# Kernel tuning notes

Hardware: AMD Instinct MI355X
Metric: run time of the kernel (lower is better)

Reference implementation:

```python
import jax, jax.numpy as jnp
import numpy as np

N_NODES = 100000
N_EDGES = 1600000
IN_FEATS, HID_FEATS, OUT_FEATS = 64, 64, 32


def setup_inputs() -> dict:
    key = jax.random.key(0)
    ks = jax.random.split(key, 8)
    x = jax.random.normal(ks[0], (N_NODES, IN_FEATS), dtype=jnp.float32)
    edge_index = jax.random.randint(ks[1], (2, N_EDGES), 0, N_NODES, dtype=jnp.int64)
    s1 = 1.0 / np.sqrt(IN_FEATS)
    s2 = 1.0 / np.sqrt(HID_FEATS)
    return {
        "x": x,
        "edge_index": edge_index,
        "W1l": jax.random.uniform(ks[2], (IN_FEATS, HID_FEATS), jnp.float32, -s1, s1),
        "W1r": jax.random.uniform(ks[3], (IN_FEATS, HID_FEATS), jnp.float32, -s1, s1),
        "b1": jnp.zeros((HID_FEATS,), jnp.float32),
        "W2l": jax.random.uniform(ks[4], (HID_FEATS, OUT_FEATS), jnp.float32, -s2, s2),
        "W2r": jax.random.uniform(ks[5], (HID_FEATS, OUT_FEATS), jnp.float32, -s2, s2),
        "b2": jnp.zeros((OUT_FEATS,), jnp.float32),
    }


def _mean_aggregate(h, src, dst, n_nodes):
    # gather source features, scatter-mean into destination nodes
    msg_sum = jax.ops.segment_sum(h[src], dst, num_segments=n_nodes)  # [N, D]
    cnt = jax.ops.segment_sum(jnp.ones(src.shape, h.dtype), dst, num_segments=n_nodes)
    return msg_sum / jnp.maximum(cnt, 1.0)[:, None]  # zero in-degree -> 0


def _sage_conv(h, src, dst, Wl, Wr, b):
    # PyG SAGEConv: lin_l(mean_j x_j) + lin_r(x_i); bias lives in lin_l
    agg = _mean_aggregate(h, src, dst, h.shape[0])
    return agg @ Wl + h @ Wr + b


def reference(x, edge_index, W1l, W1r, b1, W2l, W2r, b2):
    src, dst = edge_index[0], edge_index[1]
    h = jax.nn.relu(_sage_conv(x, src, dst, W1l, W1r, b1))
    out = _sage_conv(h, src, dst, W2l, W2r, b2)
    return out
```

## Files before the change

### kernel.cpp

```cpp
#include <hip/hip_runtime.h>

#define NN 100000
#define NE 1600000
#define NBK 392
#define CAPB 6144
#define CVTB 6250

typedef __attribute__((ext_vector_type(8))) short bf16x8;
typedef __attribute__((ext_vector_type(4))) float f32x4;

__device__ __forceinline__ unsigned short f2b(float f) {
  unsigned b = __float_as_uint(f);
  unsigned r = b + 0x7FFF + ((b >> 16) & 1);
  return (unsigned short)(r >> 16);
}

__global__ void k_zero(int* __restrict__ g) {
  if (threadIdx.x < NBK) g[threadIdx.x] = 0;
}

__global__ void k_pre(const float* __restrict__ x, unsigned short* __restrict__ xb,
                      const float* __restrict__ W1l, const float* __restrict__ W1r,
                      unsigned short* __restrict__ WT1,
                      const float* __restrict__ W2l, const float* __restrict__ W2r,
                      unsigned short* __restrict__ WT2,
                      const int* __restrict__ src, const int* __restrict__ dst,
                      int* __restrict__ gcur, unsigned* __restrict__ pairbuf) {
  __shared__ int hist[NBK];
  __shared__ int sc[512];
  __shared__ int base[NBK], lofs[NBK];
  __shared__ unsigned epk[4096];
  __shared__ unsigned short ebk[4096];
  int t = threadIdx.x;
  int b = blockIdx.x;
  if (b < CVTB) {
    int i = (b * 256 + t) * 4;
    float4 v = *(const float4*)(x + i);
    ushort4 o;
    o.x = f2b(v.x); o.y = f2b(v.y); o.z = f2b(v.z); o.w = f2b(v.w);
    *(ushort4*)(xb + i) = o;
    return;
  }
  if (b == CVTB) {
    for (int i = t; i < 64 * 128; i += 256) {
      int f = i >> 7, k = i & 127;
      WT1[i] = f2b((k < 64) ? W1l[k * 64 + f] : W1r[(k - 64) * 64 + f]);
    }
    return;
  }
  if (b == CVTB + 1) {
    for (int i = t; i < 32 * 128; i += 256) {
      int f = i >> 7, k = i & 127;
      WT2[i] = f2b((k < 64) ? W2l[k * 32 + f] : W2r[(k - 64) * 32 + f]);
    }
    return;
  }
  int pb = b - (CVTB + 2);
  for (int i = t; i < NBK; i += 256) { hist[i] = 0; lofs[i] = 0; }
  __syncthreads();
  unsigned pk[16]; int bk[16];
  int e0 = pb * 4096 + t;
#pragma unroll
  for (int j = 0; j < 16; ++j) {
    int e = e0 + j * 256;
    if (e < NE) {
      int d = dst[e], s = src[e];
      bk[j] = d >> 8;
      pk[j] = ((unsigned)s << 8) | (unsigned)(d & 255);
      atomicAdd(&hist[bk[j]], 1);
    } else bk[j] = -1;
  }
  __syncthreads();
  sc[t] = (t < NBK) ? hist[t] : 0;
  sc[t + 256] = (t + 256 < NBK) ? hist[t + 256] : 0;
  __syncthreads();
  for (int off = 1; off < 512; off <<= 1) {
    int v0 = (t >= off) ? sc[t - off] : 0;
    int v1 = sc[t + 256 - off];
    __syncthreads();
    sc[t] += v0;
    sc[t + 256] += v1;
    __syncthreads();
  }
  for (int i = t; i < NBK; i += 256) {
    int h = hist[i];
    base[i] = atomicAdd(&gcur[i], h);
    hist[i] = sc[i] - h;
  }
  __syncthreads();
#pragma unroll
  for (int j = 0; j < 16; ++j) {
    if (bk[j] >= 0) {
      int pos = hist[bk[j]] + atomicAdd(&lofs[bk[j]], 1);
      epk[pos] = pk[j];
      ebk[pos] = (unsigned short)bk[j];
    }
  }
  __syncthreads();
  int cb = sc[511];
  for (int i = t; i < cb; i += 256) {
    unsigned p = epk[i];
    int bb = ebk[i];
    int slot = base[bb] + (i - hist[bb]);
    if (slot < CAPB) pairbuf[(size_t)bb * CAPB + slot] = p;
  }
}

__global__ void k_partB(const unsigned* __restrict__ pairbuf, const int* __restrict__ gcur,
                        int* __restrict__ esrc, uint2* __restrict__ rowp2) {
  __shared__ int cnt[256], cur[256], ssum[256];
  __shared__ int ebuf[CAPB];
  int b = blockIdx.x, t = threadIdx.x;
  int cb = gcur[b]; if (cb > CAPB) cb = CAPB;
  if (t < 256) cnt[t] = 0;
  __syncthreads();
  const unsigned* pb = pairbuf + (size_t)b * CAPB;
  for (int i = t; i < cb; i += 512) atomicAdd(&cnt[pb[i] & 255], 1);
  __syncthreads();
  int a0 = (t < 256) ? cnt[t] : 0;
  if (t < 256) ssum[t] = a0;
  __syncthreads();
  for (int off = 1; off < 256; off <<= 1) {
    int tmp = (t < 256 && t >= off) ? ssum[t - off] : 0;
    __syncthreads();
    if (t < 256) ssum[t] += tmp;
    __syncthreads();
  }
  if (t < 256) {
    int ex = ssum[t] - a0;
    cur[t] = ex;
    int n = b * 256 + t;
    if (n < NN) rowp2[n] = make_uint2((unsigned)(b * CAPB + ex),
                                      (unsigned)(b * CAPB + ex + a0));
  }
  __syncthreads();
  for (int i = t; i < cb; i += 512) {
    unsigned p = pb[i];
    int pos = atomicAdd(&cur[p & 255], 1);
    ebuf[pos] = (int)(p >> 8);
  }
  __syncthreads();
  for (int i = t; i < cb; i += 512) esrc[(size_t)b * CAPB + i] = ebuf[i];
}

__global__ __launch_bounds__(256, 4) void k_agg(
    const uint2* __restrict__ fb64, const uint2* __restrict__ rowp2,
    const int* __restrict__ esrc, uint2* __restrict__ aggb64) {
  int tid = blockIdx.x * 256 + threadIdx.x;
  int node = tid >> 4;
  int c16 = tid & 15;
  int qbase = threadIdx.x & 48;
  unsigned long long rp =
      __builtin_nontemporal_load((const unsigned long long*)&rowp2[node]);
  int beg = (int)(unsigned)rp;
  int deg = (int)(unsigned)(rp >> 32) - beg;
  float a0 = 0.f, a1 = 0.f, a2 = 0.f, a3 = 0.f;

  int nfull = deg & ~15;
  for (int r0 = 0; r0 < nfull; r0 += 16) {
    int idxv = __builtin_nontemporal_load(&esrc[beg + r0 + c16]);
    int sv[16];
#pragma unroll
    for (int j = 0; j < 16; ++j) sv[j] = __shfl(idxv, qbase + j);
    uint2 v[16];
#pragma unroll
    for (int j = 0; j < 16; ++j) v[j] = fb64[(size_t)sv[j] * 16 + c16];
    __builtin_amdgcn_sched_barrier(0);
#pragma unroll
    for (int j = 0; j < 16; ++j) {
      a0 += __uint_as_float(v[j].x << 16);
      a1 += __uint_as_float(v[j].x & 0xFFFF0000u);
      a2 += __uint_as_float(v[j].y << 16);
      a3 += __uint_as_float(v[j].y & 0xFFFF0000u);
    }
  }
  int rem = deg - nfull;
  if (rem) {
    int idxv = __builtin_nontemporal_load(&esrc[beg + nfull + (c16 < rem ? c16 : 0)]);
    int sv[16];
#pragma unroll
    for (int j = 0; j < 16; ++j) sv[j] = __shfl(idxv, qbase + j);
    uint2 v[16];
#pragma unroll
    for (int j = 0; j < 16; ++j)
      if (j < rem) v[j] = fb64[(size_t)sv[j] * 16 + c16];
    __builtin_amdgcn_sched_barrier(0);
#pragma unroll
    for (int j = 0; j < 16; ++j)
      if (j < rem) {
        a0 += __uint_as_float(v[j].x << 16);
        a1 += __uint_as_float(v[j].x & 0xFFFF0000u);
        a2 += __uint_as_float(v[j].y << 16);
        a3 += __uint_as_float(v[j].y & 0xFFFF0000u);
      }
  }
  float inv = (deg > 0) ? (1.0f / (float)deg) : 0.f;
  uint2 o;
  o.x = (unsigned)f2b(a0 * inv) | ((unsigned)f2b(a1 * inv) << 16);
  o.y = (unsigned)f2b(a2 * inv) | ((unsigned)f2b(a3 * inv) << 16);
  aggb64[(size_t)node * 16 + c16] = o;
}

template <int NF>
__global__ __launch_bounds__(256) void k_gemm(
    const unsigned short* __restrict__ aggb, const unsigned short* __restrict__ featb,
    const unsigned short* __restrict__ WT, const float* __restrict__ bias,
    float* __restrict__ out, unsigned short* __restrict__ ob, int relu) {
  __shared__ unsigned short As[64 * 128];
  __shared__ unsigned short Ws[NF * 128];
  int tid = threadIdx.x;
  int n0 = blockIdx.x * 64;
  int lane = tid & 63, wr = tid >> 6;

  for (int cch = tid; cch < 64 * 16; cch += 256) {
    int r = cch >> 4, s = cch & 15;
    int n = n0 + r;
    bf16x8 v = {0, 0, 0, 0, 0, 0, 0, 0};
    if (n < NN) {
      const unsigned short* p = (s < 8) ? (aggb + (size_t)n * 64 + s * 8)
                                        : (featb + (size_t)n * 64 + (s - 8) * 8);
      v = *(const bf16x8*)p;
    }
    *(bf16x8*)(&As[r * 128 + ((s ^ (r & 15)) << 3)]) = v;
  }
  for (int cch = tid; cch < NF * 16; cch += 256) {
    int f = cch >> 4, s = cch & 15;
    bf16x8 v = *(const bf16x8*)(WT + f * 128 + s * 8);
    *(bf16x8*)(&Ws[f * 128 + ((s ^ (f & 15)) << 3)]) = v;
  }
  __syncthreads();

  int l15 = lane & 15, lg = lane >> 4;
  int arow = wr * 16 + l15;
  f32x4 acc[NF / 16];
#pragma unroll
  for (int ct = 0; ct < NF / 16; ++ct) acc[ct] = (f32x4){0.f, 0.f, 0.f, 0.f};

#pragma unroll
  for (int k0 = 0; k0 < 4; ++k0) {
    int sa = k0 * 4 + lg;
    bf16x8 a = *(const bf16x8*)(&As[arow * 128 + ((sa ^ (arow & 15)) << 3)]);
#pragma unroll
    for (int ct = 0; ct < NF / 16; ++ct) {
      int bcol = ct * 16 + l15;
      bf16x8 b = *(const bf16x8*)(&Ws[bcol * 128 + ((sa ^ (bcol & 15)) << 3)]);
      acc[ct] = __builtin_amdgcn_mfma_f32_16x16x32_bf16(a, b, acc[ct], 0, 0, 0);
    }
  }

#pragma unroll
  for (int ct = 0; ct < NF / 16; ++ct) {
    int f = ct * 16 + l15;
    float bv = bias[f];
#pragma unroll
    for (int r = 0; r < 4; ++r) {
      int n = n0 + wr * 16 + lg * 4 + r;
      if (n >= NN) continue;
      float v = acc[ct][r] + bv;
      if (relu) v = fmaxf(v, 0.f);
      if (out) out[(size_t)n * NF + f] = v;
      if (ob) ob[(size_t)n * NF + f] = f2b(v);
    }
  }
}

extern "C" void kernel_launch(void* const* d_in, const int* in_sizes, int n_in,
                              void* d_out, int out_size, void* d_ws, size_t ws_size,
                              hipStream_t stream) {
  const float* x   = (const float*)d_in[0];
  const int*   ei  = (const int*)d_in[1];
  const float* W1l = (const float*)d_in[2];
  const float* W1r = (const float*)d_in[3];
  const float* b1  = (const float*)d_in[4];
  const float* W2l = (const float*)d_in[5];
  const float* W2r = (const float*)d_in[6];
  const float* b2  = (const float*)d_in[7];
  const int* src = ei;
  const int* dst = ei + NE;
  float* out = (float*)d_out;

  char* ws = (char*)d_ws;
  size_t off = 0;
  auto take = [&](size_t bytes) -> char* {
    char* p = ws + off;
    off = (off + bytes + 255) & ~(size_t)255;
    return p;
  };
  int*      gcur    = (int*)take((size_t)NBK * 4);
  unsigned* pairbuf = (unsigned*)take((size_t)NBK * CAPB * 4);
  int*      esrc    = (int*)take((size_t)NBK * CAPB * 4);
  uint2*    rowp2   = (uint2*)take((size_t)NN * 8);
  unsigned short* aggb = (unsigned short*)take((size_t)NN * 64 * 2);
  unsigned short* xb   = (unsigned short*)take((size_t)NN * 64 * 2);
  unsigned short* hb   = (unsigned short*)take((size_t)NN * 64 * 2);
  unsigned short* WT1  = (unsigned short*)take((size_t)64 * 128 * 2);
  unsigned short* WT2  = (unsigned short*)take((size_t)32 * 128 * 2);

  int nbA = (NE + 4095) / 4096;
  k_zero<<<1, 512, 0, stream>>>(gcur);
  k_pre<<<CVTB + 2 + nbA, 256, 0, stream>>>(x, xb, W1l, W1r, WT1, W2l, W2r, WT2,
                                            src, dst, gcur, pairbuf);
  k_partB<<<NBK, 512, 0, stream>>>(pairbuf, gcur, esrc, rowp2);

  int nbG = (NN + 63) / 64;
  k_agg<<<NN / 16, 256, 0, stream>>>((const uint2*)xb, rowp2, esrc, (uint2*)aggb);
  k_gemm<64><<<nbG, 256, 0, stream>>>(aggb, xb, WT1, b1, nullptr, hb, 1);
  k_agg<<<NN / 16, 256, 0, stream>>>((const uint2*)hb, rowp2, esrc, (uint2*)aggb);
  k_gemm<32><<<nbG, 256, 0, stream>>>(aggb, hb, WT2, b2, out, nullptr, 0);
}
```

Measured before the change: 131.0 us.

## Split bf16 feature tables into two 32-column slabs for cache-friendly gathers

Measured after the change: 159.0 us. 21.4% more time.

```diff
diff --git a/kernel.cpp b/kernel.cpp
--- a/kernel.cpp
+++ b/kernel.cpp
@@ -5,6 +5,7 @@
 #define NBK 392
 #define CAPB 6144
 #define CVTB 6250
+#define SLABU (NN * 32)
 
 typedef __attribute__((ext_vector_type(8))) short bf16x8;
 typedef __attribute__((ext_vector_type(4))) float f32x4;
@@ -35,10 +36,11 @@
   int b = blockIdx.x;
   if (b < CVTB) {
     int i = (b * 256 + t) * 4;
+    int n = i >> 6, f = i & 63;
     float4 v = *(const float4*)(x + i);
     ushort4 o;
     o.x = f2b(v.x); o.y = f2b(v.y); o.z = f2b(v.z); o.w = f2b(v.w);
-    *(ushort4*)(xb + i) = o;
+    *(ushort4*)(xb + (size_t)(f >> 5) * SLABU + (size_t)n * 32 + (f & 31)) = o;
     return;
   }
   if (b == CVTB) {
@@ -144,30 +146,30 @@
 }
 
 __global__ __launch_bounds__(256, 4) void k_agg(
-    const uint2* __restrict__ fb64, const uint2* __restrict__ rowp2,
-    const int* __restrict__ esrc, uint2* __restrict__ aggb64) {
+    const uint2* __restrict__ slab_fb, const uint2* __restrict__ rowp2,
+    const int* __restrict__ esrc, uint2* __restrict__ slab_out) {
   int tid = blockIdx.x * 256 + threadIdx.x;
-  int node = tid >> 4;
-  int c16 = tid & 15;
-  int qbase = threadIdx.x & 48;
+  int node = tid >> 3;
+  int c8 = tid & 7;
+  int gbase = threadIdx.x & 56;
   unsigned long long rp =
       __builtin_nontemporal_load((const unsigned long long*)&rowp2[node]);
   int beg = (int)(unsigned)rp;
   int deg = (int)(unsigned)(rp >> 32) - beg;
   float a0 = 0.f, a1 = 0.f, a2 = 0.f, a3 = 0.f;
 
-  int nfull = deg & ~15;
-  for (int r0 = 0; r0 < nfull; r0 += 16) {
-    int idxv = __builtin_nontemporal_load(&esrc[beg + r0 + c16]);
-    int sv[16];
-#pragma unroll
-    for (int j = 0; j < 16; ++j) sv[j] = __shfl(idxv, qbase + j);
-    uint2 v[16];
-#pragma unroll
-    for (int j = 0; j < 16; ++j) v[j] = fb64[(size_t)sv[j] * 16 + c16];
+  int nfull = deg & ~7;
+  for (int r0 = 0; r0 < nfull; r0 += 8) {
+    int idxv = __builtin_nontemporal_load(&esrc[beg + r0 + c8]);
+    int sv[8];
+#pragma unroll
+    for (int j = 0; j < 8; ++j) sv[j] = __shfl(idxv, gbase + j);
+    uint2 v[8];
+#pragma unroll
+    for (int j = 0; j < 8; ++j) v[j] = slab_fb[(size_t)sv[j] * 8 + c8];
     __builtin_amdgcn_sched_barrier(0);
 #pragma unroll
-    for (int j = 0; j < 16; ++j) {
+    for (int j = 0; j < 8; ++j) {
       a0 += __uint_as_float(v[j].x << 16);
       a1 += __uint_as_float(v[j].x & 0xFFFF0000u);
       a2 += __uint_as_float(v[j].y << 16);
@@ -176,17 +178,17 @@
   }
   int rem = deg - nfull;
   if (rem) {
-    int idxv = __builtin_nontemporal_load(&esrc[beg + nfull + (c16 < rem ? c16 : 0)]);
-    int sv[16];
-#pragma unroll
-    for (int j = 0; j < 16; ++j) sv[j] = __shfl(idxv, qbase + j);
-    uint2 v[16];
-#pragma unroll
-    for (int j = 0; j < 16; ++j)
-      if (j < rem) v[j] = fb64[(size_t)sv[j] * 16 + c16];
+    int idxv = __builtin_nontemporal_load(&esrc[beg + nfull + (c8 < rem ? c8 : 0)]);
+    int sv[8];
+#pragma unroll
+    for (int j = 0; j < 8; ++j) sv[j] = __shfl(idxv, gbase + j);
+    uint2 v[8];
+#pragma unroll
+    for (int j = 0; j < 8; ++j)
+      if (j < rem) v[j] = slab_fb[(size_t)sv[j] * 8 + c8];
     __builtin_amdgcn_sched_barrier(0);
 #pragma unroll
-    for (int j = 0; j < 16; ++j)
+    for (int j = 0; j < 8; ++j)
       if (j < rem) {
         a0 += __uint_as_float(v[j].x << 16);
         a1 += __uint_as_float(v[j].x & 0xFFFF0000u);
@@ -195,10 +197,11 @@
       }
   }
   float inv = (deg > 0) ? (1.0f / (float)deg) : 0.f;
-  uint2 o;
-  o.x = (unsigned)f2b(a0 * inv) | ((unsigned)f2b(a1 * inv) << 16);
-  o.y = (unsigned)f2b(a2 * inv) | ((unsigned)f2b(a3 * inv) << 16);
-  aggb64[(size_t)node * 16 + c16] = o;
+  unsigned lo = (unsigned)f2b(a0 * inv) | ((unsigned)f2b(a1 * inv) << 16);
+  unsigned hi = (unsigned)f2b(a2 * inv) | ((unsigned)f2b(a3 * inv) << 16);
+  unsigned long long ov = (unsigned long long)lo | ((unsigned long long)hi << 32);
+  __builtin_nontemporal_store(ov,
+      (unsigned long long*)(slab_out + (size_t)node * 8 + c8));
 }
 
 template <int NF>
@@ -217,9 +220,11 @@
     int n = n0 + r;
     bf16x8 v = {0, 0, 0, 0, 0, 0, 0, 0};
     if (n < NN) {
-      const unsigned short* p = (s < 8) ? (aggb + (size_t)n * 64 + s * 8)
-                                        : (featb + (size_t)n * 64 + (s - 8) * 8);
-      v = *(const bf16x8*)p;
+      int s8 = s & 7;
+      const unsigned short* p = ((s < 8) ? aggb : featb) +
+          (size_t)(s8 >> 2) * SLABU + (size_t)n * 32 + (s8 & 3) * 8;
+      v = (s < 8) ? __builtin_nontemporal_load((const bf16x8*)p)
+                  : *(const bf16x8*)p;
     }
     *(bf16x8*)(&As[r * 128 + ((s ^ (r & 15)) << 3)]) = v;
   }
@@ -259,7 +264,7 @@
       float v = acc[ct][r] + bv;
       if (relu) v = fmaxf(v, 0.f);
       if (out) out[(size_t)n * NF + f] = v;
-      if (ob) ob[(size_t)n * NF + f] = f2b(v);
+      if (ob) ob[(size_t)(f >> 5) * SLABU + (size_t)n * 32 + (f & 31)] = f2b(v);
     }
   }
 }
@@ -303,8 +308,13 @@
   k_partB<<<NBK, 512, 0, stream>>>(pairbuf, gcur, esrc, rowp2);
 
   int nbG = (NN + 63) / 64;
-  k_agg<<<NN / 16, 256, 0, stream>>>((const uint2*)xb, rowp2, esrc, (uint2*)aggb);
+  int nbS = (NN * 8) / 256;
+  k_agg<<<nbS, 256, 0, stream>>>((const uint2*)xb, rowp2, esrc, (uint2*)aggb);
+  k_agg<<<nbS, 256, 0, stream>>>((const uint2*)xb + (size_t)NN * 8, rowp2, esrc,
+                                 (uint2*)aggb + (size_t)NN * 8);
   k_gemm<64><<<nbG, 256, 0, stream>>>(aggb, xb, WT1, b1, nullptr, hb, 1);
-  k_agg<<<NN / 16, 256, 0, stream>>>((const uint2*)hb, rowp2, esrc, (uint2*)aggb);
+  k_agg<<<nbS, 256, 0, stream>>>((const uint2*)hb, rowp2, esrc, (uint2*)aggb);
+  k_agg<<<nbS, 256, 0, stream>>>((const uint2*)hb + (size_t)NN * 8, rowp2, esrc,
+                                 (uint2*)aggb + (size_t)NN * 8);
   k_gemm<32><<<nbG, 256, 0, stream>>>(aggb, hb, WT2, b2, out, nullptr, 0);
 }
```
